# Performance work log

Measured on AMD Instinct MI355X. Metric: run time of the kernel, lower is better.

The kernel has to match this reference:

```python
import jax, jax.numpy as jnp
import numpy as np

B, N, C = 64, 1700, 256
E_SP, E_TM = 6400, 10000


def gcn_conv(x, W, b, edge_index, num_nodes):
    """PyG GCNConv (normalize=True, add_self_loops=True) on batched [B,N,C] input,
    gathering/scattering along the node axis (node_dim=-2)."""
    row, col = edge_index[0], edge_index[1]
    loops = jnp.arange(num_nodes, dtype=row.dtype)
    row = jnp.concatenate([row, loops])
    col = jnp.concatenate([col, loops])
    w = jnp.ones(row.shape[0], dtype=x.dtype)
    deg = jax.ops.segment_sum(w, col, num_segments=num_nodes)
    dinv = jnp.where(deg > 0, jax.lax.rsqrt(deg), jnp.zeros_like(deg))
    norm = dinv[row] * dinv[col]                      # [E+N]
    h = x @ W                                         # [B,N,Cout]
    msg = h[:, row, :] * norm[None, :, None]          # gather along joints
    out = jnp.zeros((x.shape[0], num_nodes, W.shape[1]), x.dtype)
    out = out.at[:, col, :].add(msg)                  # scatter-add along joints
    return out + b


def setup_inputs() -> dict:
    key = jax.random.key(0)
    ks = jax.random.split(key, 9)
    s = 1.0 / np.sqrt(C)
    return {
        "x": jax.random.normal(ks[0], (B, N, C), jnp.float32),
        "W1": jax.random.uniform(ks[1], (C, C), jnp.float32, -s, s),
        "b1": jnp.zeros((C,), jnp.float32),
        "W2": jax.random.uniform(ks[2], (C, C), jnp.float32, -s, s),
        "b2": jnp.zeros((C,), jnp.float32),
        "W3": jax.random.uniform(ks[3], (C, C), jnp.float32, -s, s),
        "b3": jnp.zeros((C,), jnp.float32),
        "keypoint_line_without_temporal": jax.random.randint(ks[4], (2, E_SP), 0, N, jnp.int32),
        "keypoint_line_with_temporal": jax.random.randint(ks[5], (2, E_TM), 0, N, jnp.int32),
    }


def reference(x, W1, b1, W2, b2, W3, b3,
              keypoint_line_without_temporal, keypoint_line_with_temporal):
    num_nodes = x.shape[1]
    residual = x  # downsample is None -> identity residual
    out = jax.nn.relu(gcn_conv(x, W1, b1, keypoint_line_without_temporal, num_nodes))
    out = jax.nn.relu(gcn_conv(out, W2, b2, keypoint_line_with_temporal, num_nodes))
    out = gcn_conv(out, W3, b3, keypoint_line_without_temporal, num_nodes)
    return jax.nn.relu(out + residual)
```

## Files before the change

### kernel.cpp

```cpp
#include <hip/hip_runtime.h>

#define NNODES 1700
#define CDIM   256

typedef __attribute__((ext_vector_type(8))) short bf16x8;
typedef __attribute__((ext_vector_type(4))) float f32x4;

__device__ inline float bf2f(unsigned h) { return __uint_as_float(h << 16); }
__device__ inline unsigned short f2bf(float f) {
  unsigned u = __float_as_uint(f);
  u = (u + 0x7FFFu + ((u >> 16) & 1u)) >> 16;
  return (unsigned short)u;
}

__device__ inline void async_copy16(const void* gsrc, void* ldst) {
  __builtin_amdgcn_global_load_lds(
      (const __attribute__((address_space(1))) unsigned int*)gsrc,
      (__attribute__((address_space(3))) unsigned int*)ldst,
      16, 0, 0);
}


__global__ void zero_kernel(int* p, int n) {
  int i = blockIdx.x * blockDim.x + threadIdx.x;
  if (i < n) p[i] = 0;
}

__global__ void count_kernel(const int* __restrict__ ei, int E, int* __restrict__ cnt) {
  int i = blockIdx.x * blockDim.x + threadIdx.x;
  if (i < E) atomicAdd(&cnt[ei[E + i]], 1);
}

__global__ void dinv_kernel(const int* __restrict__ cnt, float* __restrict__ dinv, int n) {
  int i = blockIdx.x * blockDim.x + threadIdx.x;
  if (i < n) dinv[i] = rsqrtf((float)(cnt[i] + 1));
}

__global__ __launch_bounds__(1024) void scan_kernel(const int* __restrict__ cnt, int n,
                                                    int* __restrict__ off) {
  __shared__ int s[2048];
  int t = threadIdx.x;
  for (int i = t; i < 2048; i += 1024) s[i] = (i < n) ? (cnt[i] + 1) : 0;
  for (int d = 1; d < 2048; d <<= 1) {
    __syncthreads();
    int idx = (t + 1) * (d << 1) - 1;
    if (idx < 2048) s[idx] += s[idx - d];
  }
  __syncthreads();
  if (t == 0) s[2047] = 0;
  for (int d = 1024; d >= 1; d >>= 1) {
    __syncthreads();
    int idx = (t + 1) * (d << 1) - 1;
    if (idx < 2048) { int tmp = s[idx - d]; s[idx - d] = s[idx]; s[idx] += tmp; }
  }
  __syncthreads();
  for (int i = t; i <= n; i += 1024) off[i] = s[i];
}

__global__ void fill_kernel(const int* __restrict__ ei, int E, int n,
                            const float* __restrict__ dinv, const int* __restrict__ off,
                            int* __restrict__ cursor, int* __restrict__ srcv,
                            float* __restrict__ wv) {
  int i = blockIdx.x * blockDim.x + threadIdx.x;
  if (i >= E + n) return;
  int s, d;
  if (i < E) { s = ei[i]; d = ei[E + i]; } else { s = d = i - E; }
  float w = dinv[s] * dinv[d];
  int p = atomicAdd(&cursor[d], 1);
  int idx = off[d] + p;
  srcv[idx] = s;
  wv[idx] = w;
}

__global__ void transpose_kernel(const float* __restrict__ W,
                                 unsigned short* __restrict__ Wt) {
  int i = blockIdx.x * 256 + threadIdx.x;
  int k = i >> 8, n = i & 255;
  Wt[n * 256 + k] = f2bf(W[i]);
}


template <bool AF32>
__global__ __launch_bounds__(256) void gemm128(const void* __restrict__ Ap,
                                               const unsigned short* __restrict__ Wt,
                                               unsigned short* __restrict__ H) {
  __shared__ __align__(16) unsigned short As[128 * 32];
  __shared__ __align__(16) unsigned short Bs[128 * 32];
  const int m0 = blockIdx.x * 128;
  const int n0 = blockIdx.y * 128;
  const int t = threadIdx.x;
  const int lane = t & 63;
  const int w = t >> 6;
  const int wm = (w & 1) * 64;
  const int wn = (w >> 1) * 64;
  const int lr = lane & 15;
  const int lk = (lane >> 4) * 8;

  f32x4 acc[4][4] = {};

  const int q0 = t;
  const int q1 = t + 256;

  for (int k0 = 0; k0 < 256; k0 += 32) {
    if (AF32) {
      const float* A = (const float*)Ap;
      const int row = t >> 1, kh = (t & 1) * 16;
      const float* g = A + (size_t)(m0 + row) * CDIM + k0 + kh;
      float4 f0 = *(const float4*)(g + 0);
      float4 f1 = *(const float4*)(g + 4);
      float4 f2 = *(const float4*)(g + 8);
      float4 f3 = *(const float4*)(g + 12);
      unsigned short* dst = &As[row * 32 + kh];
      bf16x8 p0, p1;
      p0[0] = (short)f2bf(f0.x); p0[1] = (short)f2bf(f0.y);
      p0[2] = (short)f2bf(f0.z); p0[3] = (short)f2bf(f0.w);
      p0[4] = (short)f2bf(f1.x); p0[5] = (short)f2bf(f1.y);
      p0[6] = (short)f2bf(f1.z); p0[7] = (short)f2bf(f1.w);
      p1[0] = (short)f2bf(f2.x); p1[1] = (short)f2bf(f2.y);
      p1[2] = (short)f2bf(f2.z); p1[3] = (short)f2bf(f2.w);
      p1[4] = (short)f2bf(f3.x); p1[5] = (short)f2bf(f3.y);
      p1[6] = (short)f2bf(f3.z); p1[7] = (short)f2bf(f3.w);
      *(bf16x8*)(dst) = p0;
      *(bf16x8*)(dst + 8) = p1;
    } else {
      const unsigned short* A = (const unsigned short*)Ap;
      async_copy16(A + (size_t)(m0 + (q0 >> 2)) * CDIM + k0 + (q0 & 3) * 8, As + q0 * 8);
      async_copy16(A + (size_t)(m0 + (q1 >> 2)) * CDIM + k0 + (q1 & 3) * 8, As + q1 * 8);
    }
    async_copy16(Wt + (size_t)(n0 + (q0 >> 2)) * CDIM + k0 + (q0 & 3) * 8, Bs + q0 * 8);
    async_copy16(Wt + (size_t)(n0 + (q1 >> 2)) * CDIM + k0 + (q1 & 3) * 8, Bs + q1 * 8);
    __syncthreads();

    bf16x8 a[4], b[4];
#pragma unroll
    for (int i = 0; i < 4; i++)
      a[i] = *(const bf16x8*)&As[(wm + i * 16 + lr) * 32 + lk];
#pragma unroll
    for (int i = 0; i < 4; i++)
      b[i] = *(const bf16x8*)&Bs[(wn + i * 16 + lr) * 32 + lk];
#pragma unroll
    for (int mi = 0; mi < 4; mi++)
#pragma unroll
      for (int ni = 0; ni < 4; ni++)
        acc[mi][ni] = __builtin_amdgcn_mfma_f32_16x16x32_bf16(a[mi], b[ni], acc[mi][ni], 0, 0, 0);
    __syncthreads();
  }

  const int orow = (lane >> 4) * 4;
#pragma unroll
  for (int mi = 0; mi < 4; mi++) {
#pragma unroll
    for (int ni = 0; ni < 4; ni++) {
#pragma unroll
      for (int r = 0; r < 4; r++) {
        int gr = m0 + wm + mi * 16 + orow + r;
        int gc = n0 + wn + ni * 16 + lr;
        H[(size_t)gr * CDIM + gc] = f2bf(acc[mi][ni][r]);
      }
    }
  }
}


template <bool FINAL>
__global__ __launch_bounds__(256) void agg_kernel(const unsigned short* __restrict__ H,
                                                  const int* __restrict__ off,
                                                  const int* __restrict__ srcv,
                                                  const float* __restrict__ wv,
                                                  const float* __restrict__ bias,
                                                  const float* __restrict__ resid,
                                                  void* __restrict__ outp) {
  const int n = blockIdx.x;
  const int b = blockIdx.y * 4 + (threadIdx.x >> 6);
  const int c = (threadIdx.x & 63) * 4;
  const int beg = off[n], end = off[n + 1];

  float a0 = 0.f, a1 = 0.f, a2 = 0.f, a3 = 0.f;
  for (int i = beg; i < end; i++) {
    int s = srcv[i];
    float w = wv[i];
    uint2 v = *(const uint2*)(H + ((size_t)b * NNODES + s) * CDIM + c);
    a0 += w * bf2f(v.x & 0xffffu);
    a1 += w * bf2f(v.x >> 16);
    a2 += w * bf2f(v.y & 0xffffu);
    a3 += w * bf2f(v.y >> 16);
  }
  float4 bv = *(const float4*)(bias + c);
  a0 += bv.x; a1 += bv.y; a2 += bv.z; a3 += bv.w;

  const size_t o = ((size_t)b * NNODES + n) * CDIM + c;
  if (FINAL) {
    float4 rv = *(const float4*)(resid + o);
    a0 += rv.x; a1 += rv.y; a2 += rv.z; a3 += rv.w;
  }
  a0 = fmaxf(a0, 0.f); a1 = fmaxf(a1, 0.f); a2 = fmaxf(a2, 0.f); a3 = fmaxf(a3, 0.f);

  if (FINAL) {
    float4 ov; ov.x = a0; ov.y = a1; ov.z = a2; ov.w = a3;
    *(float4*)((float*)outp + o) = ov;
  } else {
    uint2 ov;
    ov.x = (unsigned)f2bf(a0) | ((unsigned)f2bf(a1) << 16);
    ov.y = (unsigned)f2bf(a2) | ((unsigned)f2bf(a3) << 16);
    *(uint2*)((unsigned short*)outp + o) = ov;
  }
}


extern "C" void kernel_launch(void* const* d_in, const int* in_sizes, int n_in,
                              void* d_out, int out_size, void* d_ws, size_t ws_size,
                              hipStream_t stream) {
  const float* x  = (const float*)d_in[0];
  const float* W1 = (const float*)d_in[1];
  const float* b1 = (const float*)d_in[2];
  const float* W2 = (const float*)d_in[3];
  const float* b2 = (const float*)d_in[4];
  const float* W3 = (const float*)d_in[5];
  const float* b3 = (const float*)d_in[6];
  const int* esp = (const int*)d_in[7];
  const int* etm = (const int*)d_in[8];

  const int Esp = in_sizes[7] / 2;
  const int Etm = in_sizes[8] / 2;
  const int B = in_sizes[0] / (NNODES * CDIM);
  const int M = B * NNODES;

  char* ws = (char*)d_ws;
  size_t woff = 0;
  auto alloc = [&](size_t bytes) -> void* {
    void* p = ws + woff;
    woff = (woff + bytes + 255) & ~(size_t)255;
    return p;
  };

  unsigned short* H   = (unsigned short*)alloc((size_t)M * CDIM * 2);
  unsigned short* Act = (unsigned short*)alloc((size_t)M * CDIM * 2);
  unsigned short* Wt  = (unsigned short*)alloc((size_t)3 * CDIM * CDIM * 2);
  int* zero_base = (int*)alloc((size_t)4 * NNODES * sizeof(int));
  int* cnt_sp = zero_base;
  int* cur_sp = zero_base + NNODES;
  int* cnt_tm = zero_base + 2 * NNODES;
  int* cur_tm = zero_base + 3 * NNODES;
  int* off_sp = (int*)alloc((NNODES + 1) * sizeof(int));
  int* off_tm = (int*)alloc((NNODES + 1) * sizeof(int));
  float* dinv_sp = (float*)alloc(NNODES * sizeof(float));
  float* dinv_tm = (float*)alloc(NNODES * sizeof(float));
  int*   src_sp = (int*)alloc((size_t)(Esp + NNODES) * sizeof(int));
  float* wgt_sp = (float*)alloc((size_t)(Esp + NNODES) * sizeof(float));
  int*   src_tm = (int*)alloc((size_t)(Etm + NNODES) * sizeof(int));
  float* wgt_tm = (float*)alloc((size_t)(Etm + NNODES) * sizeof(float));

  zero_kernel<<<(4 * NNODES + 255) / 256, 256, 0, stream>>>(zero_base, 4 * NNODES);
  transpose_kernel<<<256, 256, 0, stream>>>(W1, Wt);
  transpose_kernel<<<256, 256, 0, stream>>>(W2, Wt + CDIM * CDIM);
  transpose_kernel<<<256, 256, 0, stream>>>(W3, Wt + 2 * CDIM * CDIM);
  count_kernel<<<(Esp + 255) / 256, 256, 0, stream>>>(esp, Esp, cnt_sp);
  count_kernel<<<(Etm + 255) / 256, 256, 0, stream>>>(etm, Etm, cnt_tm);
  dinv_kernel<<<(NNODES + 255) / 256, 256, 0, stream>>>(cnt_sp, dinv_sp, NNODES);
  dinv_kernel<<<(NNODES + 255) / 256, 256, 0, stream>>>(cnt_tm, dinv_tm, NNODES);
  scan_kernel<<<1, 1024, 0, stream>>>(cnt_sp, NNODES, off_sp);
  scan_kernel<<<1, 1024, 0, stream>>>(cnt_tm, NNODES, off_tm);
  fill_kernel<<<(Esp + NNODES + 255) / 256, 256, 0, stream>>>(esp, Esp, NNODES, dinv_sp,
                                                              off_sp, cur_sp, src_sp, wgt_sp);
  fill_kernel<<<(Etm + NNODES + 255) / 256, 256, 0, stream>>>(etm, Etm, NNODES, dinv_tm,
                                                              off_tm, cur_tm, src_tm, wgt_tm);

  dim3 ggrid(M / 128, CDIM / 128);
  dim3 agrid(NNODES, B / 4);

  gemm128<true><<<ggrid, 256, 0, stream>>>(x, Wt, H);
  agg_kernel<false><<<agrid, 256, 0, stream>>>(H, off_sp, src_sp, wgt_sp, b1, nullptr, Act);
  gemm128<false><<<ggrid, 256, 0, stream>>>(Act, Wt + CDIM * CDIM, H);
  agg_kernel<false><<<agrid, 256, 0, stream>>>(H, off_tm, src_tm, wgt_tm, b2, nullptr, Act);
  gemm128<false><<<ggrid, 256, 0, stream>>>(Act, Wt + 2 * CDIM * CDIM, H);
  agg_kernel<true><<<agrid, 256, 0, stream>>>(H, off_sp, src_sp, wgt_sp, b3, x, d_out);
}
```

Measured before the change: 480.2 us.

## Fuse neighbor aggregation and GEMM into one kernel per GCN layer

Each GCN layer becomes a single kernel that first aggregates over neighbors (using linearity, A·(X·W) = (A·X)·W) into an LDS tile, then multiplies that tile by the weights with MFMA and applies bias, ReLU and the residual in the epilogue. The intermediate H buffer and its global round trip go away, as do half of the launches. The weights are pre-tiled in k-major 32-wide slabs and read directly from global memory, and LDS writes use an XOR swizzle. In exchange the gather now reads the f32 input for layer 1 and uses scattered per-thread 64-byte row reads. The 64 KB LDS tile per block also limits occupancy.

Result: slower. 687.0 us (+43.1%).

```diff
diff --git a/kernel.cpp b/kernel.cpp
--- a/kernel.cpp
+++ b/kernel.cpp
@@ -11,13 +11,6 @@
   unsigned u = __float_as_uint(f);
   u = (u + 0x7FFFu + ((u >> 16) & 1u)) >> 16;
   return (unsigned short)u;
-}
-
-__device__ inline void async_copy16(const void* gsrc, void* ldst) {
-  __builtin_amdgcn_global_load_lds(
-      (const __attribute__((address_space(1))) unsigned int*)gsrc,
-      (__attribute__((address_space(3))) unsigned int*)ldst,
-      16, 0, 0);
 }
 
 
@@ -73,136 +66,118 @@
 }
 
 __global__ void transpose_kernel(const float* __restrict__ W,
-                                 unsigned short* __restrict__ Wt) {
+                                 unsigned short* __restrict__ Wtt) {
   int i = blockIdx.x * 256 + threadIdx.x;
   int k = i >> 8, n = i & 255;
-  Wt[n * 256 + k] = f2bf(W[i]);
-}
-
-
-template <bool AF32>
-__global__ __launch_bounds__(256) void gemm128(const void* __restrict__ Ap,
-                                               const unsigned short* __restrict__ Wt,
-                                               unsigned short* __restrict__ H) {
-  __shared__ __align__(16) unsigned short As[128 * 32];
-  __shared__ __align__(16) unsigned short Bs[128 * 32];
-  const int m0 = blockIdx.x * 128;
-  const int n0 = blockIdx.y * 128;
+  Wtt[(((k >> 5) << 8) + n) * 32 + (k & 31)] = f2bf(W[i]);
+}
+
+
+template <bool SRC_F32, bool FINAL>
+__global__ __launch_bounds__(256, 2) void gcn_layer(
+    const void* __restrict__ Src, const unsigned short* __restrict__ Wtt,
+    const int* __restrict__ off, const int* __restrict__ srcv,
+    const float* __restrict__ wv, const float* __restrict__ bias,
+    const float* __restrict__ resid, void* __restrict__ Out) {
+  __shared__ __align__(16) unsigned short As[8 * 128 * 32];
   const int t = threadIdx.x;
-  const int lane = t & 63;
-  const int w = t >> 6;
-  const int wm = (w & 1) * 64;
-  const int wn = (w >> 1) * 64;
-  const int lr = lane & 15;
-  const int lk = (lane >> 4) * 8;
-
-  f32x4 acc[4][4] = {};
-
-  const int q0 = t;
-  const int q1 = t + 256;
-
-  for (int k0 = 0; k0 < 256; k0 += 32) {
-    if (AF32) {
-      const float* A = (const float*)Ap;
-      const int row = t >> 1, kh = (t & 1) * 16;
-      const float* g = A + (size_t)(m0 + row) * CDIM + k0 + kh;
-      float4 f0 = *(const float4*)(g + 0);
-      float4 f1 = *(const float4*)(g + 4);
-      float4 f2 = *(const float4*)(g + 8);
-      float4 f3 = *(const float4*)(g + 12);
-      unsigned short* dst = &As[row * 32 + kh];
-      bf16x8 p0, p1;
-      p0[0] = (short)f2bf(f0.x); p0[1] = (short)f2bf(f0.y);
-      p0[2] = (short)f2bf(f0.z); p0[3] = (short)f2bf(f0.w);
-      p0[4] = (short)f2bf(f1.x); p0[5] = (short)f2bf(f1.y);
-      p0[6] = (short)f2bf(f1.z); p0[7] = (short)f2bf(f1.w);
-      p1[0] = (short)f2bf(f2.x); p1[1] = (short)f2bf(f2.y);
-      p1[2] = (short)f2bf(f2.z); p1[3] = (short)f2bf(f2.w);
-      p1[4] = (short)f2bf(f3.x); p1[5] = (short)f2bf(f3.y);
-      p1[6] = (short)f2bf(f3.z); p1[7] = (short)f2bf(f3.w);
-      *(bf16x8*)(dst) = p0;
-      *(bf16x8*)(dst + 8) = p1;
-    } else {
-      const unsigned short* A = (const unsigned short*)Ap;
-      async_copy16(A + (size_t)(m0 + (q0 >> 2)) * CDIM + k0 + (q0 & 3) * 8, As + q0 * 8);
-      async_copy16(A + (size_t)(m0 + (q1 >> 2)) * CDIM + k0 + (q1 & 3) * 8, As + q1 * 8);
-    }
-    async_copy16(Wt + (size_t)(n0 + (q0 >> 2)) * CDIM + k0 + (q0 & 3) * 8, Bs + q0 * 8);
-    async_copy16(Wt + (size_t)(n0 + (q1 >> 2)) * CDIM + k0 + (q1 & 3) * 8, Bs + q1 * 8);
-    __syncthreads();
-
-    bf16x8 a[4], b[4];
-#pragma unroll
-    for (int i = 0; i < 4; i++)
-      a[i] = *(const bf16x8*)&As[(wm + i * 16 + lr) * 32 + lk];
-#pragma unroll
-    for (int i = 0; i < 4; i++)
-      b[i] = *(const bf16x8*)&Bs[(wn + i * 16 + lr) * 32 + lk];
-#pragma unroll
-    for (int mi = 0; mi < 4; mi++)
-#pragma unroll
-      for (int ni = 0; ni < 4; ni++)
-        acc[mi][ni] = __builtin_amdgcn_mfma_f32_16x16x32_bf16(a[mi], b[ni], acc[mi][ni], 0, 0, 0);
-    __syncthreads();
-  }
-
-  const int orow = (lane >> 4) * 4;
+  const int row0 = blockIdx.x * 128;
+
+#pragma unroll
+  for (int j = 0; j < 4; j++) {
+    const int s = ((t >> 4) & 3) | ((j & 1) << 2);
+    const int r = (t & 15) | (((t >> 6) & 3) << 4) | ((j >> 1) << 6);
+    const int grow = row0 + r;
+    const int b = grow / NNODES;
+    const int n = grow - b * NNODES;
+    const int beg = off[n], end = off[n + 1];
+    float acc[32];
+#pragma unroll
+    for (int c = 0; c < 32; c++) acc[c] = 0.f;
+    for (int e = beg; e < end; e++) {
+      const int sr = b * NNODES + srcv[e];
+      const float w = wv[e];
+      if (SRC_F32) {
+        const float* p = (const float*)Src + (size_t)sr * CDIM + s * 32;
+#pragma unroll
+        for (int c4 = 0; c4 < 8; c4++) {
+          float4 v = *(const float4*)(p + c4 * 4);
+          acc[c4 * 4 + 0] += w * v.x; acc[c4 * 4 + 1] += w * v.y;
+          acc[c4 * 4 + 2] += w * v.z; acc[c4 * 4 + 3] += w * v.w;
+        }
+      } else {
+        const unsigned short* p = (const unsigned short*)Src + (size_t)sr * CDIM + s * 32;
+#pragma unroll
+        for (int c8 = 0; c8 < 4; c8++) {
+          uint4 v = *(const uint4*)(p + c8 * 8);
+          acc[c8 * 8 + 0] += w * bf2f(v.x & 0xffffu); acc[c8 * 8 + 1] += w * bf2f(v.x >> 16);
+          acc[c8 * 8 + 2] += w * bf2f(v.y & 0xffffu); acc[c8 * 8 + 3] += w * bf2f(v.y >> 16);
+          acc[c8 * 8 + 4] += w * bf2f(v.z & 0xffffu); acc[c8 * 8 + 5] += w * bf2f(v.z >> 16);
+          acc[c8 * 8 + 6] += w * bf2f(v.w & 0xffffu); acc[c8 * 8 + 7] += w * bf2f(v.w >> 16);
+        }
+      }
+    }
+    unsigned short* base = &As[((s << 7) + r) << 5];
+#pragma unroll
+    for (int u = 0; u < 4; u++) {
+      const int pu = u ^ (r & 3);
+      bf16x8 pk;
+#pragma unroll
+      for (int c = 0; c < 8; c++) pk[c] = (short)f2bf(acc[u * 8 + c]);
+      *(bf16x8*)(base + (pu << 3)) = pk;
+    }
+  }
+  __syncthreads();
+
+  const int lane = t & 63, w = t >> 6;
+  const int wm = (w & 1) * 64, wn = (w >> 1) * 128;
+  const int rl = lane & 15, q = lane >> 4;
+  f32x4 acc[4][8];
+#pragma unroll
+  for (int mi = 0; mi < 4; mi++)
+#pragma unroll
+    for (int ni = 0; ni < 8; ni++) acc[mi][ni] = (f32x4){0.f, 0.f, 0.f, 0.f};
+
+  const int swq = (q ^ (rl & 3)) << 3;
+  for (int s = 0; s < 8; s++) {
+    bf16x8 a[4];
+#pragma unroll
+    for (int mi = 0; mi < 4; mi++) {
+      const int r = wm + mi * 16 + rl;
+      a[mi] = *(const bf16x8*)&As[(((s << 7) + r) << 5) + swq];
+    }
+#pragma unroll
+    for (int ni = 0; ni < 8; ni++) {
+      const int n = wn + ni * 16 + rl;
+      bf16x8 bfr = *(const bf16x8*)&Wtt[((s << 8) + n) * 32 + (q << 3)];
+#pragma unroll
+      for (int mi = 0; mi < 4; mi++)
+        acc[mi][ni] = __builtin_amdgcn_mfma_f32_16x16x32_bf16(a[mi], bfr, acc[mi][ni], 0, 0, 0);
+    }
+  }
+
+  float bv[8];
+#pragma unroll
+  for (int ni = 0; ni < 8; ni++) bv[ni] = bias[wn + ni * 16 + rl];
+  const int orow = q * 4;
 #pragma unroll
   for (int mi = 0; mi < 4; mi++) {
 #pragma unroll
-    for (int ni = 0; ni < 4; ni++) {
-#pragma unroll
-      for (int r = 0; r < 4; r++) {
-        int gr = m0 + wm + mi * 16 + orow + r;
-        int gc = n0 + wn + ni * 16 + lr;
-        H[(size_t)gr * CDIM + gc] = f2bf(acc[mi][ni][r]);
+    for (int ni = 0; ni < 8; ni++) {
+      const int col = wn + ni * 16 + rl;
+#pragma unroll
+      for (int rr = 0; rr < 4; rr++) {
+        const int grow = row0 + wm + mi * 16 + orow + rr;
+        const size_t o = (size_t)grow * CDIM + col;
+        float v = acc[mi][ni][rr] + bv[ni];
+        if (FINAL) {
+          v += resid[o];
+          ((float*)Out)[o] = fmaxf(v, 0.f);
+        } else {
+          ((unsigned short*)Out)[o] = f2bf(fmaxf(v, 0.f));
+        }
       }
     }
-  }
-}
-
-
-template <bool FINAL>
-__global__ __launch_bounds__(256) void agg_kernel(const unsigned short* __restrict__ H,
-                                                  const int* __restrict__ off,
-                                                  const int* __restrict__ srcv,
-                                                  const float* __restrict__ wv,
-                                                  const float* __restrict__ bias,
-                                                  const float* __restrict__ resid,
-                                                  void* __restrict__ outp) {
-  const int n = blockIdx.x;
-  const int b = blockIdx.y * 4 + (threadIdx.x >> 6);
-  const int c = (threadIdx.x & 63) * 4;
-  const int beg = off[n], end = off[n + 1];
-
-  float a0 = 0.f, a1 = 0.f, a2 = 0.f, a3 = 0.f;
-  for (int i = beg; i < end; i++) {
-    int s = srcv[i];
-    float w = wv[i];
-    uint2 v = *(const uint2*)(H + ((size_t)b * NNODES + s) * CDIM + c);
-    a0 += w * bf2f(v.x & 0xffffu);
-    a1 += w * bf2f(v.x >> 16);
-    a2 += w * bf2f(v.y & 0xffffu);
-    a3 += w * bf2f(v.y >> 16);
-  }
-  float4 bv = *(const float4*)(bias + c);
-  a0 += bv.x; a1 += bv.y; a2 += bv.z; a3 += bv.w;
-
-  const size_t o = ((size_t)b * NNODES + n) * CDIM + c;
-  if (FINAL) {
-    float4 rv = *(const float4*)(resid + o);
-    a0 += rv.x; a1 += rv.y; a2 += rv.z; a3 += rv.w;
-  }
-  a0 = fmaxf(a0, 0.f); a1 = fmaxf(a1, 0.f); a2 = fmaxf(a2, 0.f); a3 = fmaxf(a3, 0.f);
-
-  if (FINAL) {
-    float4 ov; ov.x = a0; ov.y = a1; ov.z = a2; ov.w = a3;
-    *(float4*)((float*)outp + o) = ov;
-  } else {
-    uint2 ov;
-    ov.x = (unsigned)f2bf(a0) | ((unsigned)f2bf(a1) << 16);
-    ov.y = (unsigned)f2bf(a2) | ((unsigned)f2bf(a3) << 16);
-    *(uint2*)((unsigned short*)outp + o) = ov;
   }
 }
 
@@ -233,9 +208,9 @@
     return p;
   };
 
-  unsigned short* H   = (unsigned short*)alloc((size_t)M * CDIM * 2);
-  unsigned short* Act = (unsigned short*)alloc((size_t)M * CDIM * 2);
-  unsigned short* Wt  = (unsigned short*)alloc((size_t)3 * CDIM * CDIM * 2);
+  unsigned short* Act1 = (unsigned short*)alloc((size_t)M * CDIM * 2);
+  unsigned short* Act2 = (unsigned short*)alloc((size_t)M * CDIM * 2);
+  unsigned short* Wtt  = (unsigned short*)alloc((size_t)3 * CDIM * CDIM * 2);
   int* zero_base = (int*)alloc((size_t)4 * NNODES * sizeof(int));
   int* cnt_sp = zero_base;
   int* cur_sp = zero_base + NNODES;
@@ -251,9 +226,9 @@
   float* wgt_tm = (float*)alloc((size_t)(Etm + NNODES) * sizeof(float));
 
   zero_kernel<<<(4 * NNODES + 255) / 256, 256, 0, stream>>>(zero_base, 4 * NNODES);
-  transpose_kernel<<<256, 256, 0, stream>>>(W1, Wt);
-  transpose_kernel<<<256, 256, 0, stream>>>(W2, Wt + CDIM * CDIM);
-  transpose_kernel<<<256, 256, 0, stream>>>(W3, Wt + 2 * CDIM * CDIM);
+  transpose_kernel<<<256, 256, 0, stream>>>(W1, Wtt);
+  transpose_kernel<<<256, 256, 0, stream>>>(W2, Wtt + CDIM * CDIM);
+  transpose_kernel<<<256, 256, 0, stream>>>(W3, Wtt + 2 * CDIM * CDIM);
   count_kernel<<<(Esp + 255) / 256, 256, 0, stream>>>(esp, Esp, cnt_sp);
   count_kernel<<<(Etm + 255) / 256, 256, 0, stream>>>(etm, Etm, cnt_tm);
   dinv_kernel<<<(NNODES + 255) / 256, 256, 0, stream>>>(cnt_sp, dinv_sp, NNODES);
@@ -265,13 +240,12 @@
   fill_kernel<<<(Etm + NNODES + 255) / 256, 256, 0, stream>>>(etm, Etm, NNODES, dinv_tm,
                                                               off_tm, cur_tm, src_tm, wgt_tm);
 
-  dim3 ggrid(M / 128, CDIM / 128);
-  dim3 agrid(NNODES, B / 4);
-
-  gemm128<true><<<ggrid, 256, 0, stream>>>(x, Wt, H);
-  agg_kernel<false><<<agrid, 256, 0, stream>>>(H, off_sp, src_sp, wgt_sp, b1, nullptr, Act);
-  gemm128<false><<<ggrid, 256, 0, stream>>>(Act, Wt + CDIM * CDIM, H);
-  agg_kernel<false><<<agrid, 256, 0, stream>>>(H, off_tm, src_tm, wgt_tm, b2, nullptr, Act);
-  gemm128<false><<<ggrid, 256, 0, stream>>>(Act, Wt + 2 * CDIM * CDIM, H);
-  agg_kernel<true><<<agrid, 256, 0, stream>>>(H, off_sp, src_sp, wgt_sp, b3, x, d_out);
-}
+  const int nblk = M / 128;
+
+  gcn_layer<true, false><<<nblk, 256, 0, stream>>>(x, Wtt, off_sp, src_sp, wgt_sp, b1,
+                                                   nullptr, Act1);
+  gcn_layer<false, false><<<nblk, 256, 0, stream>>>(Act1, Wtt + CDIM * CDIM, off_tm, src_tm,
+                                                    wgt_tm, b2, nullptr, Act2);
+  gcn_layer<false, true><<<nblk, 256, 0, stream>>>(Act2, Wtt + 2 * CDIM * CDIM, off_sp,
+                                                   src_sp, wgt_sp, b3, x, d_out);
+}
```

## Use node-major activation layout, full-N GEMM tiles, and prefetch in aggregation

Applied to the files above, without the earlier changes.

Intermediate activations H/Act now use a node-major [N][B][C] layout, so the aggregation's gathers for a node read contiguous batch rows. The GEMM is rewritten to load a whole 128x256 A tile into LDS once and compute all 256 output columns per block. B fragments are read directly from a k-blocked pre-transposed weight in global memory instead of being staged through LDS. The aggregation loop software-pipelines the next edge's load. The cost is a 64KB LDS tile and a large accumulator set per thread, which may limit occupancy, and the batch size is now hardcoded to 64.

Result: slower. 510.5 us (+6.3%).

```diff
diff --git a/kernel.cpp b/kernel.cpp
--- a/kernel.cpp
+++ b/kernel.cpp
@@ -2,6 +2,7 @@
 
 #define NNODES 1700
 #define CDIM   256
+#define NB     64
 
 typedef __attribute__((ext_vector_type(8))) short bf16x8;
 typedef __attribute__((ext_vector_type(4))) float f32x4;
@@ -73,89 +74,85 @@
 }
 
 __global__ void transpose_kernel(const float* __restrict__ W,
-                                 unsigned short* __restrict__ Wt) {
+                                 unsigned short* __restrict__ Wtt) {
   int i = blockIdx.x * 256 + threadIdx.x;
   int k = i >> 8, n = i & 255;
-  Wt[n * 256 + k] = f2bf(W[i]);
+  Wtt[(((k >> 5) << 8) + n) * 32 + (k & 31)] = f2bf(W[i]);
 }
 
 
 template <bool AF32>
-__global__ __launch_bounds__(256) void gemm128(const void* __restrict__ Ap,
-                                               const unsigned short* __restrict__ Wt,
-                                               unsigned short* __restrict__ H) {
-  __shared__ __align__(16) unsigned short As[128 * 32];
-  __shared__ __align__(16) unsigned short Bs[128 * 32];
-  const int m0 = blockIdx.x * 128;
-  const int n0 = blockIdx.y * 128;
+__global__ __launch_bounds__(256, 2) void gemm_fullN(const void* __restrict__ Ap,
+                                                     const unsigned short* __restrict__ Wtt,
+                                                     unsigned short* __restrict__ H) {
+  __shared__ __align__(16) unsigned short As[8 * 128 * 32];
   const int t = threadIdx.x;
-  const int lane = t & 63;
-  const int w = t >> 6;
-  const int wm = (w & 1) * 64;
-  const int wn = (w >> 1) * 64;
-  const int lr = lane & 15;
-  const int lk = (lane >> 4) * 8;
-
-  f32x4 acc[4][4] = {};
-
-  const int q0 = t;
-  const int q1 = t + 256;
-
-  for (int k0 = 0; k0 < 256; k0 += 32) {
-    if (AF32) {
-      const float* A = (const float*)Ap;
-      const int row = t >> 1, kh = (t & 1) * 16;
-      const float* g = A + (size_t)(m0 + row) * CDIM + k0 + kh;
-      float4 f0 = *(const float4*)(g + 0);
-      float4 f1 = *(const float4*)(g + 4);
-      float4 f2 = *(const float4*)(g + 8);
-      float4 f3 = *(const float4*)(g + 12);
-      unsigned short* dst = &As[row * 32 + kh];
-      bf16x8 p0, p1;
-      p0[0] = (short)f2bf(f0.x); p0[1] = (short)f2bf(f0.y);
-      p0[2] = (short)f2bf(f0.z); p0[3] = (short)f2bf(f0.w);
-      p0[4] = (short)f2bf(f1.x); p0[5] = (short)f2bf(f1.y);
-      p0[6] = (short)f2bf(f1.z); p0[7] = (short)f2bf(f1.w);
-      p1[0] = (short)f2bf(f2.x); p1[1] = (short)f2bf(f2.y);
-      p1[2] = (short)f2bf(f2.z); p1[3] = (short)f2bf(f2.w);
-      p1[4] = (short)f2bf(f3.x); p1[5] = (short)f2bf(f3.y);
-      p1[6] = (short)f2bf(f3.z); p1[7] = (short)f2bf(f3.w);
-      *(bf16x8*)(dst) = p0;
-      *(bf16x8*)(dst + 8) = p1;
-    } else {
-      const unsigned short* A = (const unsigned short*)Ap;
-      async_copy16(A + (size_t)(m0 + (q0 >> 2)) * CDIM + k0 + (q0 & 3) * 8, As + q0 * 8);
-      async_copy16(A + (size_t)(m0 + (q1 >> 2)) * CDIM + k0 + (q1 & 3) * 8, As + q1 * 8);
-    }
-    async_copy16(Wt + (size_t)(n0 + (q0 >> 2)) * CDIM + k0 + (q0 & 3) * 8, Bs + q0 * 8);
-    async_copy16(Wt + (size_t)(n0 + (q1 >> 2)) * CDIM + k0 + (q1 & 3) * 8, Bs + q1 * 8);
-    __syncthreads();
-
-    bf16x8 a[4], b[4];
-#pragma unroll
-    for (int i = 0; i < 4; i++)
-      a[i] = *(const bf16x8*)&As[(wm + i * 16 + lr) * 32 + lk];
-#pragma unroll
-    for (int i = 0; i < 4; i++)
-      b[i] = *(const bf16x8*)&Bs[(wn + i * 16 + lr) * 32 + lk];
+  const int row0 = blockIdx.x * 128;
+
+  if (AF32) {
+    const float* A = (const float*)Ap;
+#pragma unroll
+    for (int j = 0; j < 16; j++) {
+      const int c = t + j * 256;
+      const int u = c & 3, row = (c >> 2) & 127, s = c >> 9;
+      const int g = row0 + row;
+      const int n = g >> 6, b = g & (NB - 1);
+      const float* src = A + ((size_t)b * NNODES + n) * CDIM + s * 32 + u * 8;
+      float4 f0 = *(const float4*)src;
+      float4 f1 = *(const float4*)(src + 4);
+      bf16x8 pk;
+      pk[0] = (short)f2bf(f0.x); pk[1] = (short)f2bf(f0.y);
+      pk[2] = (short)f2bf(f0.z); pk[3] = (short)f2bf(f0.w);
+      pk[4] = (short)f2bf(f1.x); pk[5] = (short)f2bf(f1.y);
+      pk[6] = (short)f2bf(f1.z); pk[7] = (short)f2bf(f1.w);
+      *(bf16x8*)((char*)As + (size_t)c * 16) = pk;
+    }
+  } else {
+    const unsigned short* A = (const unsigned short*)Ap;
+#pragma unroll
+    for (int j = 0; j < 16; j++) {
+      const int c = t + j * 256;
+      const int u = c & 3, row = (c >> 2) & 127, s = c >> 9;
+      async_copy16(A + (size_t)(row0 + row) * CDIM + s * 32 + u * 8,
+                   (char*)As + (size_t)c * 16);
+    }
+  }
+  __syncthreads();
+
+  const int lane = t & 63, w = t >> 6;
+  const int wm = (w & 1) * 64, wn = (w >> 1) * 128;
+  const int rl = lane & 15, q = lane >> 4;
+  f32x4 acc[4][8];
+#pragma unroll
+  for (int mi = 0; mi < 4; mi++)
+#pragma unroll
+    for (int ni = 0; ni < 8; ni++) acc[mi][ni] = (f32x4){0.f, 0.f, 0.f, 0.f};
+
+#pragma unroll
+  for (int s = 0; s < 8; s++) {
+    bf16x8 a[4];
 #pragma unroll
     for (int mi = 0; mi < 4; mi++)
-#pragma unroll
-      for (int ni = 0; ni < 4; ni++)
-        acc[mi][ni] = __builtin_amdgcn_mfma_f32_16x16x32_bf16(a[mi], b[ni], acc[mi][ni], 0, 0, 0);
-    __syncthreads();
-  }
-
-  const int orow = (lane >> 4) * 4;
+      a[mi] = *(const bf16x8*)((char*)As + s * 8192 + (wm + mi * 16 + rl) * 64 + q * 16);
+#pragma unroll
+    for (int ni = 0; ni < 8; ni++) {
+      bf16x8 bfr = *(const bf16x8*)&Wtt[((s << 8) + wn + ni * 16 + rl) * 32 + (q << 3)];
+#pragma unroll
+      for (int mi = 0; mi < 4; mi++)
+        acc[mi][ni] = __builtin_amdgcn_mfma_f32_16x16x32_bf16(a[mi], bfr, acc[mi][ni], 0, 0, 0);
+    }
+  }
+
+  const int orow = q * 4;
 #pragma unroll
   for (int mi = 0; mi < 4; mi++) {
 #pragma unroll
-    for (int ni = 0; ni < 4; ni++) {
-#pragma unroll
-      for (int r = 0; r < 4; r++) {
-        int gr = m0 + wm + mi * 16 + orow + r;
-        int gc = n0 + wn + ni * 16 + lr;
-        H[(size_t)gr * CDIM + gc] = f2bf(acc[mi][ni][r]);
+    for (int ni = 0; ni < 8; ni++) {
+      const int col = wn + ni * 16 + rl;
+#pragma unroll
+      for (int rr = 0; rr < 4; rr++) {
+        const int grow = row0 + wm + mi * 16 + orow + rr;
+        H[(size_t)grow * CDIM + col] = f2bf(acc[mi][ni][rr]);
       }
     }
   }
@@ -174,31 +171,40 @@
   const int b = blockIdx.y * 4 + (threadIdx.x >> 6);
   const int c = (threadIdx.x & 63) * 4;
   const int beg = off[n], end = off[n + 1];
+  const unsigned short* Hb = H + (size_t)b * CDIM + c;
 
   float a0 = 0.f, a1 = 0.f, a2 = 0.f, a3 = 0.f;
-  for (int i = beg; i < end; i++) {
-    int s = srcv[i];
-    float w = wv[i];
-    uint2 v = *(const uint2*)(H + ((size_t)b * NNODES + s) * CDIM + c);
+  int sr = srcv[beg];
+  float w = wv[beg];
+  uint2 v = *(const uint2*)(Hb + (size_t)sr * (NB * CDIM));
+  for (int e = beg + 1; e < end; e++) {
+    int sr1 = srcv[e];
+    float w1 = wv[e];
+    uint2 v1 = *(const uint2*)(Hb + (size_t)sr1 * (NB * CDIM));
     a0 += w * bf2f(v.x & 0xffffu);
     a1 += w * bf2f(v.x >> 16);
     a2 += w * bf2f(v.y & 0xffffu);
     a3 += w * bf2f(v.y >> 16);
-  }
+    w = w1; v = v1;
+  }
+  a0 += w * bf2f(v.x & 0xffffu);
+  a1 += w * bf2f(v.x >> 16);
+  a2 += w * bf2f(v.y & 0xffffu);
+  a3 += w * bf2f(v.y >> 16);
+
   float4 bv = *(const float4*)(bias + c);
   a0 += bv.x; a1 += bv.y; a2 += bv.z; a3 += bv.w;
 
-  const size_t o = ((size_t)b * NNODES + n) * CDIM + c;
   if (FINAL) {
+    const size_t o = ((size_t)b * NNODES + n) * CDIM + c;
     float4 rv = *(const float4*)(resid + o);
-    a0 += rv.x; a1 += rv.y; a2 += rv.z; a3 += rv.w;
-  }
-  a0 = fmaxf(a0, 0.f); a1 = fmaxf(a1, 0.f); a2 = fmaxf(a2, 0.f); a3 = fmaxf(a3, 0.f);
-
-  if (FINAL) {
+    a0 = fmaxf(a0 + rv.x, 0.f); a1 = fmaxf(a1 + rv.y, 0.f);
+    a2 = fmaxf(a2 + rv.z, 0.f); a3 = fmaxf(a3 + rv.w, 0.f);
     float4 ov; ov.x = a0; ov.y = a1; ov.z = a2; ov.w = a3;
     *(float4*)((float*)outp + o) = ov;
   } else {
+    const size_t o = ((size_t)n * NB + b) * CDIM + c;
+    a0 = fmaxf(a0, 0.f); a1 = fmaxf(a1, 0.f); a2 = fmaxf(a2, 0.f); a3 = fmaxf(a3, 0.f);
     uint2 ov;
     ov.x = (unsigned)f2bf(a0) | ((unsigned)f2bf(a1) << 16);
     ov.y = (unsigned)f2bf(a2) | ((unsigned)f2bf(a3) << 16);
@@ -222,8 +228,7 @@
 
   const int Esp = in_sizes[7] / 2;
   const int Etm = in_sizes[8] / 2;
-  const int B = in_sizes[0] / (NNODES * CDIM);
-  const int M = B * NNODES;
+  const int M = NB * NNODES;
 
   char* ws = (char*)d_ws;
   size_t woff = 0;
@@ -235,7 +240,7 @@
 
   unsigned short* H   = (unsigned short*)alloc((size_t)M * CDIM * 2);
   unsigned short* Act = (unsigned short*)alloc((size_t)M * CDIM * 2);
-  unsigned short* Wt  = (unsigned short*)alloc((size_t)3 * CDIM * CDIM * 2);
+  unsigned short* Wtt = (unsigned short*)alloc((size_t)3 * CDIM * CDIM * 2);
   int* zero_base = (int*)alloc((size_t)4 * NNODES * sizeof(int));
   int* cnt_sp = zero_base;
   int* cur_sp = zero_base + NNODES;
@@ -251,9 +256,9 @@
   float* wgt_tm = (float*)alloc((size_t)(Etm + NNODES) * sizeof(float));
 
   zero_kernel<<<(4 * NNODES + 255) / 256, 256, 0, stream>>>(zero_base, 4 * NNODES);
-  transpose_kernel<<<256, 256, 0, stream>>>(W1, Wt);
-  transpose_kernel<<<256, 256, 0, stream>>>(W2, Wt + CDIM * CDIM);
-  transpose_kernel<<<256, 256, 0, stream>>>(W3, Wt + 2 * CDIM * CDIM);
+  transpose_kernel<<<256, 256, 0, stream>>>(W1, Wtt);
+  transpose_kernel<<<256, 256, 0, stream>>>(W2, Wtt + CDIM * CDIM);
+  transpose_kernel<<<256, 256, 0, stream>>>(W3, Wtt + 2 * CDIM * CDIM);
   count_kernel<<<(Esp + 255) / 256, 256, 0, stream>>>(esp, Esp, cnt_sp);
   count_kernel<<<(Etm + 255) / 256, 256, 0, stream>>>(etm, Etm, cnt_tm);
   dinv_kernel<<<(NNODES + 255) / 256, 256, 0, stream>>>(cnt_sp, dinv_sp, NNODES);
@@ -265,13 +270,13 @@
   fill_kernel<<<(Etm + NNODES + 255) / 256, 256, 0, stream>>>(etm, Etm, NNODES, dinv_tm,
                                                               off_tm, cur_tm, src_tm, wgt_tm);
 
-  dim3 ggrid(M / 128, CDIM / 128);
-  dim3 agrid(NNODES, B / 4);
-
-  gemm128<true><<<ggrid, 256, 0, stream>>>(x, Wt, H);
+  const int nblk = M / 128;
+  dim3 agrid(NNODES, NB / 4);
+
+  gemm_fullN<true><<<nblk, 256, 0, stream>>>(x, Wtt, H);
   agg_kernel<false><<<agrid, 256, 0, stream>>>(H, off_sp, src_sp, wgt_sp, b1, nullptr, Act);
-  gemm128<false><<<ggrid, 256, 0, stream>>>(Act, Wt + CDIM * CDIM, H);
+  gemm_fullN<false><<<nblk, 256, 0, stream>>>(Act, Wtt + CDIM * CDIM, H);
   agg_kernel<false><<<agrid, 256, 0, stream>>>(H, off_tm, src_tm, wgt_tm, b2, nullptr, Act);
-  gemm128<false><<<ggrid, 256, 0, stream>>>(Act, Wt + 2 * CDIM * CDIM, H);
+  gemm_fullN<false><<<nblk, 256, 0, stream>>>(Act, Wtt + 2 * CDIM * CDIM, H);
   agg_kernel<true><<<agrid, 256, 0, stream>>>(H, off_sp, src_sp, wgt_sp, b3, x, d_out);
 }
```
